# Performance work log

Measured on AMD Instinct MI355X. Metric: run time of the kernel, lower is better.

Reference implementation:

```python
import jax, jax.numpy as jnp
import numpy as np

K = 16  # top-k, matches init kwarg k


def _topk_weighted_mean(conn, parent, k):
    """conn: [n, p] weights, parent: [p, d] -> [n, d].
    Faithful to original: argsort()[-k:] top-k, softmax over selected weights,
    then weighted sum of gathered parent rows."""
    idx = jnp.argsort(conn, axis=-1)[:, -k:]                      # [n, k]
    w = jax.nn.softmax(jnp.take_along_axis(conn, idx, axis=-1), axis=-1)  # [n, k]
    return jnp.einsum('nk,nkd->nd', w, parent[idx])               # gather + small matmul


def setup_inputs() -> dict:
    key = jax.random.key(0)
    k_ids, k_c1, k_c2, k_c3, k_root = jax.random.split(key, 5)
    objNum, clusterNums, embedDim = 200000, (1024, 256, 64), 64
    batch = 8192
    return {
        'ids': jax.random.randint(k_ids, (batch,), 0, objNum, dtype=jnp.int64)
               if jax.config.jax_enable_x64 else jax.random.randint(k_ids, (batch,), 0, objNum, dtype=jnp.int32),
        'conn1': jax.random.normal(k_c1, (objNum, clusterNums[0]), jnp.float32),
        'conn2': jax.random.normal(k_c2, (clusterNums[0], clusterNums[1]), jnp.float32),
        'conn3': jax.random.normal(k_c3, (clusterNums[1], clusterNums[2]), jnp.float32),
        'rootMatrix': jax.random.normal(k_root, (clusterNums[2], embedDim), jnp.float32),
    }


def reference(ids, conn1, conn2, conn3, rootMatrix):
    # getEmbedByLevel(2): combine rootMatrix rows -> level-2 cluster embeddings
    e2 = _topk_weighted_mean(conn3, rootMatrix, K)   # [256, d]
    # getEmbedByLevel(1): combine level-2 embeddings -> level-1 cluster embeddings
    e1 = _topk_weighted_mean(conn2, e2, K)           # [1024, d]
    # getEmbed(ids): combine level-1 embeddings per requested leaf object
    return _topk_weighted_mean(conn1[ids], e1, K)    # [B, d]
```

## Files before the change

kernel.cpp:

```cpp
#include <hip/hip_runtime.h>
#include <stdint.h>
#include <math.h>

#define WAVE 64
#define TOPK 16

__device__ __forceinline__ uint32_t f2s(float f) {
    uint32_t u = __float_as_uint(f);
    return u ^ (uint32_t)(((int32_t)u >> 31) | 0x80000000u);
}
__device__ __forceinline__ uint32_t umax32(uint32_t a, uint32_t b) { return a > b ? a : b; }
__device__ __forceinline__ uint32_t umin32(uint32_t a, uint32_t b) { return a < b ? a : b; }

template <int CTRL, int RMASK>
__device__ __forceinline__ uint32_t dppmax(uint32_t m) {
    uint32_t r = (uint32_t)__builtin_amdgcn_update_dpp((int)m, (int)m, CTRL, RMASK, 0xF, false);
    return umax32(m, r);
}

__device__ __forceinline__ uint32_t wave_umax(uint32_t m) {
    m = dppmax<0x121, 0xF>(m);
    m = dppmax<0x122, 0xF>(m);
    m = dppmax<0x124, 0xF>(m);
    m = dppmax<0x128, 0xF>(m);
    m = dppmax<0x142, 0xA>(m);
    m = dppmax<0x143, 0xC>(m);
    return (uint32_t)__builtin_amdgcn_readlane((int)m, 63);
}

template <int VPL>
__device__ __forceinline__ uint32_t gpos(int j, int lane) {
    if constexpr (VPL == 1) return (uint32_t)lane;
    else return (uint32_t)((j >> 2) * (WAVE * 4) + lane * 4 + (j & 3));
}

template <int P>
__global__ void topk_wm_kernel(const float* __restrict__ conn,
                               const int* __restrict__ rowsel,
                               const float* __restrict__ parent,
                               float* __restrict__ out,
                               int n) {
    constexpr int VPL = P / WAVE;
    constexpr uint32_t IMASK = (uint32_t)(P - 1);
    const int lane = threadIdx.x & (WAVE - 1);
    const int row = blockIdx.x * (blockDim.x >> 6) + (threadIdx.x >> 6);
    if (row >= n) return;

    const long src_row = rowsel ? (long)rowsel[row] : (long)row;
    const float* __restrict__ crow = conn + src_row * (long)P;

    uint32_t k[VPL];
    if constexpr (VPL == 1) {
        k[0] = (f2s(crow[lane]) & ~IMASK) | (uint32_t)lane;
    } else {
#pragma unroll
        for (int c = 0; c < VPL / 4; ++c) {
            float4 f4 = *reinterpret_cast<const float4*>(crow + c * (WAVE * 4) + lane * 4);
            const uint32_t b = (uint32_t)(c * (WAVE * 4) + lane * 4);
            k[c * 4 + 0] = (f2s(f4.x) & ~IMASK) | (b + 0u);
            k[c * 4 + 1] = (f2s(f4.y) & ~IMASK) | (b + 1u);
            k[c * 4 + 2] = (f2s(f4.z) & ~IMASK) | (b + 2u);
            k[c * 4 + 3] = (f2s(f4.w) & ~IMASK) | (b + 3u);
        }
#pragma unroll
        for (int size = 2; size <= VPL; size <<= 1) {
#pragma unroll
            for (int stride = size >> 1; stride > 0; stride >>= 1) {
#pragma unroll
                for (int i = 0; i < VPL; ++i) {
                    const int j = i ^ stride;
                    if (j > i) {
                        const uint32_t a = k[i], b2 = k[j];
                        const uint32_t hi = umax32(a, b2), lo = umin32(a, b2);
                        if ((i & size) == 0) { k[i] = hi; k[j] = lo; }
                        else                 { k[i] = lo; k[j] = hi; }
                    }
                }
            }
        }
    }

    uint32_t idx[TOPK];
    uint32_t q16 = 0;
#pragma unroll
    for (int t = 0; t < TOPK; ++t) {
        const uint32_t K = wave_umax(k[0]);
        idx[t] = K & IMASK;
        if (t == TOPK - 1) q16 = K & ~IMASK;
        const bool won = (k[0] == K);
#pragma unroll
        for (int j = 0; j < VPL - 1; ++j) k[j] = won ? k[j + 1] : k[j];
        k[VPL - 1] = won ? 0u : k[VPL - 1];
    }
    const uint32_t k17 = wave_umax(k[0]);

    if ((k17 & ~IMASK) == q16) {
        uint32_t v[VPL];
        if constexpr (VPL == 1) {
            v[0] = f2s(crow[lane]);
        } else {
#pragma unroll
            for (int c = 0; c < VPL / 4; ++c) {
                float4 f4 = *reinterpret_cast<const float4*>(crow + c * (WAVE * 4) + lane * 4);
                v[c * 4 + 0] = f2s(f4.x);
                v[c * 4 + 1] = f2s(f4.y);
                v[c * 4 + 2] = f2s(f4.z);
                v[c * 4 + 3] = f2s(f4.w);
            }
        }
#pragma unroll
        for (int t = 0; t < TOPK; ++t) {
            uint32_t m = v[0];
            int li = 0;
#pragma unroll
            for (int j = 1; j < VPL; ++j) {
                bool c = v[j] >= m;
                m = c ? v[j] : m;
                li = c ? j : li;
            }
            uint32_t gi = gpos<VPL>(li, lane);
            const uint32_t mygi = gi;
            uint32_t mm = m;
#pragma unroll
            for (int off = 32; off > 0; off >>= 1) {
                uint32_t om = (uint32_t)__shfl_xor((int)mm, off);
                uint32_t og = (uint32_t)__shfl_xor((int)gi, off);
                bool c = (om > mm) || (om == mm && og > gi);
                mm = c ? om : mm;
                gi = c ? og : gi;
            }
            idx[t] = gi;
            const bool won = (mygi == gi) && (m == mm);
#pragma unroll
            for (int j = 0; j < VPL; ++j) {
                if (won && j == li) v[j] = 0u;
            }
        }
    }

    float vsel[TOPK];
#pragma unroll
    for (int t = 0; t < TOPK; ++t) vsel[t] = crow[idx[t]];
    const float v0 = vsel[0];
    float ssum = 0.f, acc = 0.f;
#pragma unroll
    for (int t = 0; t < TOPK; ++t) {
        const float w = __expf(vsel[t] - v0);
        ssum += w;
        acc = fmaf(w, parent[idx[t] * 64u + (uint32_t)lane], acc);
    }
    out[(long)row * 64 + lane] = acc / ssum;
}

extern "C" void kernel_launch(void* const* d_in, const int* in_sizes, int n_in,
                              void* d_out, int out_size, void* d_ws, size_t ws_size,
                              hipStream_t stream) {
    const int* ids = (const int*)d_in[0];
    const float* conn1 = (const float*)d_in[1];
    const float* conn2 = (const float*)d_in[2];
    const float* conn3 = (const float*)d_in[3];
    const float* root = (const float*)d_in[4];
    float* out = (float*)d_out;

    const int batch = in_sizes[0];
    const int n1 = 1024, n2 = 256;

    float* e2 = (float*)d_ws;
    float* e1 = e2 + (size_t)n2 * 64;

    dim3 blk(256);

    topk_wm_kernel<64><<<dim3(n2 / 4), blk, 0, stream>>>(conn3, nullptr, root, e2, n2);
    topk_wm_kernel<256><<<dim3(n1 / 4), blk, 0, stream>>>(conn2, nullptr, e2, e1, n1);
    topk_wm_kernel<1024><<<dim3(batch / 4), blk, 0, stream>>>(conn1, ids, e1, out, batch);
}
```

Baseline: 33.92 us.

## Replace serial wave-max top-16 extraction with cross-lane bitonic merge network

The sixteen sequential wave-wide max reductions with a shift-out per round are replaced by a per-lane sort followed by a butterfly of cross-lane exchanges (DPP, ds_swizzle, ds_bpermute). Each exchange step merges two sorted top-16 lists with a bitonic clean. The tie-fallback test now counts how many elements share the truncated 16th key across the wave and compares that with the count inside the selected set. This cuts the dependent reduction chain but adds many register-heavy compare-exchange operations per step, which may raise VGPR pressure.

Result: slower. 38.77 us (+14.3%).

```diff
diff --git a/kernel.cpp b/kernel.cpp
--- a/kernel.cpp
+++ b/kernel.cpp
@@ -9,23 +9,69 @@
     uint32_t u = __float_as_uint(f);
     return u ^ (uint32_t)(((int32_t)u >> 31) | 0x80000000u);
 }
+__device__ __forceinline__ float s2f(uint32_t s) {
+    uint32_t u = (s & 0x80000000u) ? (s ^ 0x80000000u) : ~s;
+    return __uint_as_float(u);
+}
 __device__ __forceinline__ uint32_t umax32(uint32_t a, uint32_t b) { return a > b ? a : b; }
 __device__ __forceinline__ uint32_t umin32(uint32_t a, uint32_t b) { return a < b ? a : b; }
 
-template <int CTRL, int RMASK>
-__device__ __forceinline__ uint32_t dppmax(uint32_t m) {
-    uint32_t r = (uint32_t)__builtin_amdgcn_update_dpp((int)m, (int)m, CTRL, RMASK, 0xF, false);
-    return umax32(m, r);
-}
-
-__device__ __forceinline__ uint32_t wave_umax(uint32_t m) {
-    m = dppmax<0x121, 0xF>(m);
-    m = dppmax<0x122, 0xF>(m);
-    m = dppmax<0x124, 0xF>(m);
-    m = dppmax<0x128, 0xF>(m);
-    m = dppmax<0x142, 0xA>(m);
-    m = dppmax<0x143, 0xC>(m);
-    return (uint32_t)__builtin_amdgcn_readlane((int)m, 63);
+__device__ __forceinline__ void ce(uint32_t& a, uint32_t& b) {
+    uint32_t hi = umax32(a, b), lo = umin32(a, b);
+    a = hi; b = lo;
+}
+
+template <int N>
+__device__ __forceinline__ void clean_desc(uint32_t* a) {
+#pragma unroll
+    for (int stride = N / 2; stride >= 1; stride >>= 1) {
+#pragma unroll
+        for (int i = 0; i < N; ++i) {
+            if ((i & stride) == 0) ce(a[i], a[i | stride]);
+        }
+    }
+}
+
+template <int N>
+__device__ __forceinline__ void sort_desc(uint32_t* a) {
+#pragma unroll
+    for (int size = 2; size <= N; size <<= 1) {
+#pragma unroll
+        for (int stride = size >> 1; stride >= 1; stride >>= 1) {
+#pragma unroll
+            for (int i = 0; i < N; ++i) {
+                const int j = i ^ stride;
+                if (j > i) {
+                    if ((i & size) == 0) ce(a[i], a[j]);
+                    else                 ce(a[j], a[i]);
+                }
+            }
+        }
+    }
+}
+
+template <int CTRL>
+__device__ __forceinline__ uint32_t dpp_mov(uint32_t x) {
+    return (uint32_t)__builtin_amdgcn_update_dpp((int)x, (int)x, CTRL, 0xF, 0xF, false);
+}
+__device__ __forceinline__ uint32_t swz16(uint32_t x) {
+    return (uint32_t)__builtin_amdgcn_ds_swizzle((int)x, 0x401F);
+}
+__device__ __forceinline__ uint32_t bperm32(int xaddr, uint32_t x) {
+    return (uint32_t)__builtin_amdgcn_ds_bpermute(xaddr, (int)x);
+}
+
+__device__ __forceinline__ void merge_top16(uint32_t* a, const uint32_t* r) {
+#pragma unroll
+    for (int i = 0; i < 16; ++i) a[i] = umax32(a[i], r[15 - i]);
+    clean_desc<16>(a);
+}
+
+template <int L>
+__device__ __forceinline__ void merge_grow(uint32_t* a, const uint32_t* r) {
+#pragma unroll
+    for (int i = 0; i < L; ++i) a[L + i] = r[L - 1 - i];
+    clean_desc<2 * L>(a);
 }
 
 template <int VPL>
@@ -49,52 +95,102 @@
     const long src_row = rowsel ? (long)rowsel[row] : (long)row;
     const float* __restrict__ crow = conn + src_row * (long)P;
 
-    uint32_t k[VPL];
+    uint32_t a[16];
+    uint32_t b[VPL];
+
     if constexpr (VPL == 1) {
-        k[0] = (f2s(crow[lane]) & ~IMASK) | (uint32_t)lane;
+        b[0] = (f2s(crow[lane]) & ~IMASK) | (uint32_t)lane;
+        a[0] = b[0];
     } else {
 #pragma unroll
         for (int c = 0; c < VPL / 4; ++c) {
             float4 f4 = *reinterpret_cast<const float4*>(crow + c * (WAVE * 4) + lane * 4);
-            const uint32_t b = (uint32_t)(c * (WAVE * 4) + lane * 4);
-            k[c * 4 + 0] = (f2s(f4.x) & ~IMASK) | (b + 0u);
-            k[c * 4 + 1] = (f2s(f4.y) & ~IMASK) | (b + 1u);
-            k[c * 4 + 2] = (f2s(f4.z) & ~IMASK) | (b + 2u);
-            k[c * 4 + 3] = (f2s(f4.w) & ~IMASK) | (b + 3u);
-        }
-#pragma unroll
-        for (int size = 2; size <= VPL; size <<= 1) {
-#pragma unroll
-            for (int stride = size >> 1; stride > 0; stride >>= 1) {
-#pragma unroll
-                for (int i = 0; i < VPL; ++i) {
-                    const int j = i ^ stride;
-                    if (j > i) {
-                        const uint32_t a = k[i], b2 = k[j];
-                        const uint32_t hi = umax32(a, b2), lo = umin32(a, b2);
-                        if ((i & size) == 0) { k[i] = hi; k[j] = lo; }
-                        else                 { k[i] = lo; k[j] = hi; }
-                    }
-                }
-            }
-        }
-    }
-
-    uint32_t idx[TOPK];
-    uint32_t q16 = 0;
-#pragma unroll
-    for (int t = 0; t < TOPK; ++t) {
-        const uint32_t K = wave_umax(k[0]);
-        idx[t] = K & IMASK;
-        if (t == TOPK - 1) q16 = K & ~IMASK;
-        const bool won = (k[0] == K);
-#pragma unroll
-        for (int j = 0; j < VPL - 1; ++j) k[j] = won ? k[j + 1] : k[j];
-        k[VPL - 1] = won ? 0u : k[VPL - 1];
-    }
-    const uint32_t k17 = wave_umax(k[0]);
-
-    if ((k17 & ~IMASK) == q16) {
+            const uint32_t base = (uint32_t)(c * (WAVE * 4) + lane * 4);
+            b[c * 4 + 0] = (f2s(f4.x) & ~IMASK) | (base + 0u);
+            b[c * 4 + 1] = (f2s(f4.y) & ~IMASK) | (base + 1u);
+            b[c * 4 + 2] = (f2s(f4.z) & ~IMASK) | (base + 2u);
+            b[c * 4 + 3] = (f2s(f4.w) & ~IMASK) | (base + 3u);
+        }
+#pragma unroll
+        for (int j = 0; j < VPL; ++j) a[j] = b[j];
+        sort_desc<VPL>(a);
+    }
+
+    const int xaddr = (lane ^ 32) << 2;
+    uint32_t r[16];
+
+    if constexpr (VPL == 1) {
+        r[0] = bperm32(xaddr, a[0]);
+        a[1] = r[0]; clean_desc<2>(a);
+        r[0] = swz16(a[0]); r[1] = swz16(a[1]);
+        merge_grow<2>(a, r);
+#pragma unroll
+        for (int i = 0; i < 4; ++i) r[i] = dpp_mov<0x121>(a[i]);
+        merge_grow<4>(a, r);
+#pragma unroll
+        for (int i = 0; i < 8; ++i) r[i] = dpp_mov<0x122>(a[i]);
+        merge_grow<8>(a, r);
+#pragma unroll
+        for (int i = 0; i < 16; ++i) r[i] = dpp_mov<0x124>(a[i]);
+        merge_top16(a, r);
+#pragma unroll
+        for (int i = 0; i < 16; ++i) r[i] = dpp_mov<0x128>(a[i]);
+        merge_top16(a, r);
+    } else if constexpr (VPL == 4) {
+#pragma unroll
+        for (int i = 0; i < 4; ++i) r[i] = bperm32(xaddr, a[i]);
+        merge_grow<4>(a, r);
+#pragma unroll
+        for (int i = 0; i < 8; ++i) r[i] = swz16(a[i]);
+        merge_grow<8>(a, r);
+#pragma unroll
+        for (int i = 0; i < 16; ++i) r[i] = dpp_mov<0x121>(a[i]);
+        merge_top16(a, r);
+#pragma unroll
+        for (int i = 0; i < 16; ++i) r[i] = dpp_mov<0x122>(a[i]);
+        merge_top16(a, r);
+#pragma unroll
+        for (int i = 0; i < 16; ++i) r[i] = dpp_mov<0x124>(a[i]);
+        merge_top16(a, r);
+#pragma unroll
+        for (int i = 0; i < 16; ++i) r[i] = dpp_mov<0x128>(a[i]);
+        merge_top16(a, r);
+    } else {
+#pragma unroll
+        for (int i = 0; i < 16; ++i) r[i] = dpp_mov<0x121>(a[i]);
+        merge_top16(a, r);
+#pragma unroll
+        for (int i = 0; i < 16; ++i) r[i] = dpp_mov<0x122>(a[i]);
+        merge_top16(a, r);
+#pragma unroll
+        for (int i = 0; i < 16; ++i) r[i] = dpp_mov<0x124>(a[i]);
+        merge_top16(a, r);
+#pragma unroll
+        for (int i = 0; i < 16; ++i) r[i] = dpp_mov<0x128>(a[i]);
+        merge_top16(a, r);
+#pragma unroll
+        for (int i = 0; i < 16; ++i) r[i] = swz16(a[i]);
+        merge_top16(a, r);
+#pragma unroll
+        for (int i = 0; i < 16; ++i) r[i] = bperm32(xaddr, a[i]);
+        merge_top16(a, r);
+    }
+
+    const uint32_t q16 = a[15] & ~IMASK;
+    int cl = 0;
+#pragma unroll
+    for (int j = 0; j < VPL; ++j) cl += ((b[j] & ~IMASK) == q16) ? 1 : 0;
+    cl += (int)dpp_mov<0x121>((uint32_t)cl);
+    cl += (int)dpp_mov<0x122>((uint32_t)cl);
+    cl += (int)dpp_mov<0x124>((uint32_t)cl);
+    cl += (int)dpp_mov<0x128>((uint32_t)cl);
+    cl += (int)swz16((uint32_t)cl);
+    cl += (int)bperm32(xaddr, (uint32_t)cl);
+    int cs = 0;
+#pragma unroll
+    for (int t = 0; t < TOPK; ++t) cs += ((a[t] & ~IMASK) == q16) ? 1 : 0;
+
+    if (cl != cs) {
         uint32_t v[VPL];
         if constexpr (VPL == 1) {
             v[0] = f2s(crow[lane]);
@@ -129,7 +225,7 @@
                 mm = c ? om : mm;
                 gi = c ? og : gi;
             }
-            idx[t] = gi;
+            a[t] = gi;
             const bool won = (mygi == gi) && (m == mm);
 #pragma unroll
             for (int j = 0; j < VPL; ++j) {
@@ -140,14 +236,14 @@
 
     float vsel[TOPK];
 #pragma unroll
-    for (int t = 0; t < TOPK; ++t) vsel[t] = crow[idx[t]];
+    for (int t = 0; t < TOPK; ++t) vsel[t] = crow[a[t] & IMASK];
     const float v0 = vsel[0];
     float ssum = 0.f, acc = 0.f;
 #pragma unroll
     for (int t = 0; t < TOPK; ++t) {
         const float w = __expf(vsel[t] - v0);
         ssum += w;
-        acc = fmaf(w, parent[idx[t] * 64u + (uint32_t)lane], acc);
+        acc = fmaf(w, parent[(a[t] & IMASK) * 64u + (uint32_t)lane], acc);
     }
     out[(long)row * 64 + lane] = acc / ssum;
 }
```
